# Optimization experiments

Measured on AMD Instinct MI355X. Metric: run time of the kernel, lower is better.

Reference implementation:

```python
import jax, jax.numpy as jnp
import numpy as np

N, M, FEAT, GROUP, EMB = 512, 2048, 1024, 16, 64
DG = FEAT // GROUP  # 64 dims per head


def _make_boxes(k, n):
    k1, k2, k3, k4 = jax.random.split(k, 4)
    x = jax.random.uniform(k1, (n, 1)) * 800.0
    y = jax.random.uniform(k2, (n, 1)) * 800.0
    w = jax.random.uniform(k3, (n, 1)) * 120.0 + 16.0
    h = jax.random.uniform(k4, (n, 1)) * 120.0 + 16.0
    return jnp.concatenate([x, y, x + w, y + h], axis=1)


def setup_inputs() -> dict:
    key = jax.random.key(0)
    ks = jax.random.split(key, 10)
    std = 0.01
    fan = 1.0 / np.sqrt(FEAT).astype(np.float32)
    return {
        "bbox": _make_boxes(ks[0], N),
        "ref_bbox": _make_boxes(ks[1], M),
        "roi_feat": jax.random.normal(ks[2], (N, FEAT), dtype=jnp.float32),
        "ref_feat": jax.random.normal(ks[3], (M, FEAT), dtype=jnp.float32),
        "Wg_w": jax.random.normal(ks[4], (GROUP, EMB)) * std,
        "Wg_b": jnp.zeros((GROUP,), jnp.float32),
        "Wq_w": jax.random.normal(ks[5], (FEAT, FEAT)) * fan,
        "Wq_b": jnp.zeros((FEAT,), jnp.float32),
        "Wk_w": jax.random.normal(ks[6], (FEAT, FEAT)) * fan,
        "Wk_b": jnp.zeros((FEAT,), jnp.float32),
        "Wv_w": jax.random.normal(ks[7], (GROUP, DG, FEAT)) * std,
        "Wv_b": jnp.zeros((FEAT,), jnp.float32),
        "u": jax.random.normal(ks[8], (GROUP, 1, EMB)) * std,
    }


def _position_embedding(bbox, ref_bbox, feat_dim=64, wave_length=1000.0):
    # extract_position_matrix: geometry deltas between every (roi, ref) pair
    xr0, yr0, xr1, yr1 = jnp.split(ref_bbox, 4, axis=1)  # [M,1]
    wr = xr1 - xr0 + 1.0
    hr = yr1 - yr0 + 1.0
    cxr = 0.5 * (xr0 + xr1)
    cyr = 0.5 * (yr0 + yr1)
    x0, y0, x1, y1 = jnp.split(bbox, 4, axis=1)  # [N,1]
    w = x1 - x0 + 1.0
    h = y1 - y0 + 1.0
    cx = 0.5 * (x0 + x1)
    cy = 0.5 * (y0 + y1)
    dx = jnp.log(jnp.abs((cx - cxr.T) / w) + 1e-3)  # [N,M]
    dy = jnp.log(jnp.abs((cy - cyr.T) / h) + 1e-3)
    dw = jnp.log(w / wr.T)
    dh = jnp.log(h / hr.T)
    pos = jnp.stack([dx, dy, dw, dh], axis=2)  # [N,M,4]
    # extract_position_embedding: sinusoidal encoding, feat_dim/8 frequencies
    fr = jnp.arange(feat_dim // 8, dtype=pos.dtype)
    dim_mat = wave_length ** (8.0 / feat_dim * fr)  # [8]
    div = (pos[..., None] * 100.0) / dim_mat  # [N,M,4,8]
    emb = jnp.concatenate([jnp.sin(div), jnp.cos(div)], axis=3)  # [N,M,4,16]
    emb = emb.reshape(emb.shape[0], emb.shape[1], -1)  # [N,M,64]
    return jnp.transpose(emb, (2, 0, 1))  # [emb_dim, N, M]


def reference(bbox, ref_bbox, roi_feat, ref_feat, Wg_w, Wg_b, Wq_w, Wq_b,
              Wk_w, Wk_b, Wv_w, Wv_b, u):
    pe = _position_embedding(bbox, ref_bbox)  # [EMB, N, M]
    # Wg: 1x1 conv over embedding channels, relu -> attention prior weights
    pos_feat = jax.nn.relu(jnp.einsum('ge,enm->gnm', Wg_w, pe)
                           + Wg_b[:, None, None])  # [G,N,M]
    aff_weight = jnp.transpose(pos_feat, (1, 0, 2))  # [N,G,M]
    q = (roi_feat @ Wq_w.T + Wq_b).reshape(-1, GROUP, DG).transpose(1, 0, 2)  # [G,N,DG]
    k = (ref_feat @ Wk_w.T + Wk_b).reshape(-1, GROUP, DG).transpose(1, 0, 2)  # [G,M,DG]
    # content score + global content-bias (u) score, per head
    aff = jnp.einsum('gnd,gmd->gnm', q, k) + jnp.einsum('gld,gmd->glm', u, k)
    aff_scale = (aff / np.sqrt(float(DG))).transpose(1, 0, 2)  # [N,G,M]
    weighted_aff = jnp.log(aff_weight + 1e-6) + aff_scale
    attn = jax.nn.softmax(weighted_aff, axis=2)  # [N,G,M]
    out_t = jnp.einsum('ngm,mf->ngf', attn, ref_feat)  # [N,G,FEAT]
    # grouped 1x1 conv Wv: per-group weight [DG, FEAT]
    out = jnp.einsum('ngc,gdc->ngd', out_t, Wv_w).reshape(-1, FEAT) + Wv_b
    return out  # [N, FEAT]
```

## Files before the change

kernel.cpp:

```cpp
#include <hip/hip_runtime.h>
#include <stdint.h>

typedef float f32x4 __attribute__((ext_vector_type(4)));
typedef _Float16 f16x8 __attribute__((ext_vector_type(8)));
typedef _Float16 f16x4 __attribute__((ext_vector_type(4)));
typedef int int4v __attribute__((ext_vector_type(4)));

#define LOG2E 1.44269504088896340736f

__device__ __forceinline__ void gload_lds16(const void* g, void* l) {
    auto gp = reinterpret_cast<const uint32_t __attribute__((address_space(1)))*>(
        reinterpret_cast<uintptr_t>(g));
    auto lp = reinterpret_cast<uint32_t __attribute__((address_space(3)))*>(
        reinterpret_cast<uintptr_t>(l));
    __builtin_amdgcn_global_load_lds(gp, lp, 16, 0, 0);
}

__global__ __launch_bounds__(256) void mega_prep(
    const float* __restrict__ roi_feat, const float* __restrict__ ref_feat,
    const float* __restrict__ Wg_w, const float* __restrict__ Wq_w,
    const float* __restrict__ Wk_w, const float* __restrict__ Wv_w,
    _Float16* __restrict__ roi_h, _Float16* __restrict__ ref_h,
    _Float16* __restrict__ wq_h, _Float16* __restrict__ wk_h,
    _Float16* __restrict__ wv_h, _Float16* __restrict__ wg_h)
{
    int idx = blockIdx.x * 256 + threadIdx.x;
    const float* src; _Float16* dst; int off;
    if (idx < 131072)       { src = roi_feat; dst = roi_h; off = idx; }
    else if (idx < 655360)  { src = ref_feat; dst = ref_h; off = idx - 131072; }
    else if (idx < 917504)  { src = Wq_w;     dst = wq_h;  off = idx - 655360; }
    else if (idx < 1179648) { src = Wk_w;     dst = wk_h;  off = idx - 917504; }
    else if (idx < 1441792) { src = Wv_w;     dst = wv_h;  off = idx - 1179648; }
    else                    { src = Wg_w;     dst = wg_h;  off = idx - 1441792; }
    f32x4 v = *(const f32x4*)(src + (size_t)off * 4);
    f16x4 o;
    o[0] = (_Float16)v[0]; o[1] = (_Float16)v[1];
    o[2] = (_Float16)v[2]; o[3] = (_Float16)v[3];
    *(f16x4*)(dst + (size_t)off * 4) = o;
}

__global__ __launch_bounds__(256, 4) void mega_gp(
    const _Float16* __restrict__ roi_h, const _Float16* __restrict__ ref_h,
    const _Float16* __restrict__ wq_h, const _Float16* __restrict__ wk_h,
    const _Float16* __restrict__ wv_h, const _Float16* __restrict__ wg_h,
    const float* __restrict__ Wq_b, const float* __restrict__ uvec,
    const float* __restrict__ Wk_b, const float* __restrict__ Wg_b,
    const float* __restrict__ bbox, const float* __restrict__ ref_bbox,
    _Float16* __restrict__ Qg, _Float16* __restrict__ Kg, _Float16* __restrict__ Vth,
    _Float16* __restrict__ prior)
{
    __shared__ __align__(16) _Float16 As[2][4096];
    __shared__ __align__(16) _Float16 Bs[2][4096];

    int b = blockIdx.x;
    int tid = threadIdx.x;
    int w = tid >> 6, l = tid & 63, q = l >> 4, t = l & 15;

    if (b >= 1152) {
        int pb = b - 1152;
        int p = l & 15;
        int n = pb >> 1, half = pb & 1;

        f16x8 wa0 = *(const f16x8*)(wg_h + p*64 + q*8);
        f16x8 wa1 = *(const f16x8*)(wg_h + p*64 + 32 + q*8);
        f32x4 wb = *(const f32x4*)(Wg_b + q*4);

        f32x4 bbx = *(const f32x4*)(bbox + n * 4);
        float bw = bbx[2] - bbx[0] + 1.0f, bh = bbx[3] - bbx[1] + 1.0f;
        float cx = 0.5f*(bbx[0]+bbx[2]), cy = 0.5f*(bbx[1]+bbx[3]);
        float invw = 1.0f/bw, invh = 1.0f/bh;
        float lgw = __logf(bw), lgh = __logf(bh);

        float cf[8];
        #pragma unroll
        for (int f = 0; f < 8; ++f)
            cf[f] = 15.9154943091895336f * __builtin_exp2f(-1.24572303558276059f * (float)f);

        float coff = (q & 1) ? 0.25f : 0.0f;
        bool isX = (q < 2);
        float cA  = isX ? cx : cy;
        float invA = isX ? invw : invh;
        float lgA = isX ? lgw : lgh;

        int mstart = half * 1024 + w * 256;
        for (int it = 0; it < 16; ++it) {
            int m = mstart + it * 16 + p;
            f32x4 rb = *(const f32x4*)(ref_bbox + m * 4);
            float cAr = isX ? 0.5f*(rb[0]+rb[2]) : 0.5f*(rb[1]+rb[3]);
            float sAr = isX ? (rb[2]-rb[0]+1.0f) : (rb[3]-rb[1]+1.0f);
            float posA = __logf(fabsf(cA - cAr) * invA + 1e-3f);
            float posB = lgA - __logf(sAr);
            f16x8 e0, e1;
            #pragma unroll
            for (int f = 0; f < 8; ++f) {
                float a0 = posA * cf[f] + coff; a0 -= floorf(a0);
                float a1 = posB * cf[f] + coff; a1 -= floorf(a1);
                e0[f] = (_Float16)__builtin_amdgcn_sinf(a0);
                e1[f] = (_Float16)__builtin_amdgcn_sinf(a1);
            }
            f32x4 acc = wb;
            acc = __builtin_amdgcn_mfma_f32_16x16x32_f16(wa0, e0, acc, 0, 0, 0);
            acc = __builtin_amdgcn_mfma_f32_16x16x32_f16(wa1, e1, acc, 0, 0, 0);
            _Float16* pp = prior + (size_t)n * 2048 + m;
            #pragma unroll
            for (int r = 0; r < 4; ++r)
                pp[(size_t)(q*4 + r) * 1048576] = (_Float16)fmaxf(acc[r], 0.f);
        }
        return;
    }

    const _Float16 *A, *B;
    _Float16* out;
    int tm, tn, mode; float scale;
    if (b < 128)      { A = roi_h; B = wq_h; out = Qg;  tm = b >> 4;        tn = b & 15;       mode = 0; scale = 0.125f * LOG2E; }
    else if (b < 640) { A = ref_h; B = wk_h; out = Kg;  tm = (b-128) >> 4;  tn = (b-128) & 15; mode = 1; scale = 1.f; }
    else              { A = ref_h; B = wv_h; out = Vth; tm = (b-640) >> 4;  tn = (b-640) & 15; mode = 2; scale = 1.f; }
    int MR = (b < 128) ? 512 : 2048;

    int wm = w >> 1, wn = w & 1;
    int m0 = tm * 64, n0 = tn * 64;

    int r_lo = tid >> 3, c8 = tid & 7;
    int swz = (c8 * 16) ^ ((r_lo & 7) << 4);
    const char* gA = (const char*)A + (size_t)(m0 + r_lo) * 2048 + swz;
    const char* gB = (const char*)B + (size_t)(n0 + r_lo) * 2048 + swz;
    char* lA = (char*)&As[0][0] + w * 1024;
    char* lB = (char*)&Bs[0][0] + w * 1024;

#define GSTAGE(bufi, kt) { \
    size_t ko = (size_t)(kt) * 128; \
    gload_lds16(gA + ko,           lA + (bufi)*8192); \
    gload_lds16(gA + ko + 32*2048, lA + (bufi)*8192 + 4096); \
    gload_lds16(gB + ko,           lB + (bufi)*8192); \
    gload_lds16(gB + ko + 32*2048, lB + (bufi)*8192 + 4096); }

    f32x4 acc[2][2];
    #pragma unroll
    for (int i = 0; i < 2; ++i)
        #pragma unroll
        for (int j = 0; j < 2; ++j)
            acc[i][j] = (f32x4){0.f, 0.f, 0.f, 0.f};

    GSTAGE(0, 0);
    __syncthreads();

    for (int kt = 0; kt < 16; ++kt) {
        int cur = kt & 1;
        if (kt < 15) GSTAGE(cur ^ 1, kt + 1);

        const char* cA = (const char*)&As[0][0] + cur * 8192;
        const char* cB = (const char*)&Bs[0][0] + cur * 8192;
        f16x8 af[2][2], bf[2][2];
        #pragma unroll
        for (int mi = 0; mi < 2; ++mi) {
            int row = wm * 32 + mi * 16 + t;
            int sx = (row & 7) << 4;
            #pragma unroll
            for (int ks = 0; ks < 2; ++ks)
                af[ks][mi] = *(const f16x8*)(cA + row * 128 + ((ks * 64 + q * 16) ^ sx));
        }
        #pragma unroll
        for (int ni = 0; ni < 2; ++ni) {
            int row = wn * 32 + ni * 16 + t;
            int sx = (row & 7) << 4;
            #pragma unroll
            for (int ks = 0; ks < 2; ++ks)
                bf[ks][ni] = *(const f16x8*)(cB + row * 128 + ((ks * 64 + q * 16) ^ sx));
        }
        #pragma unroll
        for (int ks = 0; ks < 2; ++ks)
            #pragma unroll
            for (int mi = 0; mi < 2; ++mi)
                #pragma unroll
                for (int ni = 0; ni < 2; ++ni)
                    acc[mi][ni] = __builtin_amdgcn_mfma_f32_16x16x32_f16(af[ks][mi], bf[ks][ni], acc[mi][ni], 0, 0, 0);
        __syncthreads();
    }
#undef GSTAGE

    #pragma unroll
    for (int mi = 0; mi < 2; ++mi) {
        #pragma unroll
        for (int ni = 0; ni < 2; ++ni) {
            int col  = n0 + wn*32 + ni*16 + t;
            int row0 = m0 + wm*32 + mi*16 + q*4;
            f32x4 a = acc[mi][ni];
            if (mode == 2) {
                f16x4 pk;
                pk[0] = (_Float16)a[0]; pk[1] = (_Float16)a[1];
                pk[2] = (_Float16)a[2]; pk[3] = (_Float16)a[3];
                *(f16x4*)(out + (size_t)col * 2048 + row0) = pk;
            } else {
                float bb = (mode == 0) ? (Wq_b[col] + uvec[col]) : Wk_b[col];
                _Float16* op = out + ((size_t)(col >> 6) * MR + row0) * 64 + (col & 63);
                #pragma unroll
                for (int rr = 0; rr < 4; ++rr)
                    op[(size_t)rr * 64] = (_Float16)((a[rr] + bb) * scale);
            }
        }
    }
}

#define SWZ(row, cb) ((cb) ^ (((row) & 7) << 4))

__device__ __forceinline__ f16x8 ld128s(const _Float16* base, int row, int cb) {
    return *(const f16x8*)((const char*)base + row * 128 + SWZ(row, cb));
}
__device__ __forceinline__ f16x4 ld64s(const _Float16* base, int row, int cb) {
    return *(const f16x4*)((const char*)base + row * 128 + SWZ(row, cb));
}

__global__ __launch_bounds__(256, 3) void mega_attn(
    const _Float16* __restrict__ Qg, const _Float16* __restrict__ Kg,
    const _Float16* __restrict__ Vth, const _Float16* __restrict__ prior,
    _Float16* __restrict__ Opart, float* __restrict__ Mpart, float* __restrict__ Lpart)
{
    __shared__ __align__(16) _Float16 Kl[2][4096];
    __shared__ __align__(16) _Float16 Vl[2][4096];
    __shared__ __align__(16) _Float16 Pl[2][4096];

    int bid = blockIdx.x;
    int g = bid >> 6, nt4 = (bid >> 3) & 7, s = bid & 7;
    int tid = threadIdx.x;
    int w = tid >> 6, l = tid & 63, q = l >> 4, t = l & 15;
    int n0 = nt4 * 64, m0 = s * 256;

    int n = n0 + w * 16 + t;
    const _Float16* Qrow = Qg + ((size_t)g * 512 + n) * 64;
    f16x8 qf0 = *(const f16x8*)(Qrow + q * 8);
    f16x8 qf1 = *(const f16x8*)(Qrow + 32 + q * 8);

    int r_lo = tid >> 3, c8 = tid & 7;
    const char* gK = (const char*)(Kg + ((size_t)g * 2048 + m0) * 64);
    const char* gV = (const char*)(Vth + (size_t)g * 64 * 2048 + m0);
    const char* gP = (const char*)(prior + ((size_t)g * 512 + n0) * 2048 + m0);

    int4v kr0, kr1, vr0, vr1, pq0, pq1;
#define LOADC(c) { \
    kr0 = *(const int4v*)(gK + (c)*8192 + r_lo*128 + c8*16); \
    kr1 = *(const int4v*)(gK + (c)*8192 + (r_lo+32)*128 + c8*16); \
    vr0 = *(const int4v*)(gV + (c)*128 + (size_t)r_lo*4096 + c8*16); \
    vr1 = *(const int4v*)(gV + (c)*128 + (size_t)(r_lo+32)*4096 + c8*16); \
    pq0 = *(const int4v*)(gP + (c)*128 + (size_t)r_lo*4096 + c8*16); \
    pq1 = *(const int4v*)(gP + (c)*128 + (size_t)(r_lo+32)*4096 + c8*16); }
#define WRITEC(bufi) { \
    int cb = c8 * 16, sw = SWZ(r_lo, cb); \
    *(int4v*)((char*)&Kl[bufi][0] + r_lo*128 + sw) = kr0; \
    *(int4v*)((char*)&Kl[bufi][0] + (r_lo+32)*128 + sw) = kr1; \
    *(int4v*)((char*)&Vl[bufi][0] + r_lo*128 + sw) = vr0; \
    *(int4v*)((char*)&Vl[bufi][0] + (r_lo+32)*128 + sw) = vr1; \
    *(int4v*)((char*)&Pl[bufi][0] + r_lo*128 + sw) = pq0; \
    *(int4v*)((char*)&Pl[bufi][0] + (r_lo+32)*128 + sw) = pq1; }

    float mrow = -INFINITY, lsum = 0.f;
    f32x4 O0 = {0,0,0,0}, O1 = {0,0,0,0}, O2 = {0,0,0,0}, O3 = {0,0,0,0};

    LOADC(0);
    WRITEC(0);
    __syncthreads();

    for (int c = 0; c < 4; ++c) {
        int cur = c & 1;
        if (c < 3) LOADC(c + 1);

        const _Float16* Kb_l = &Kl[cur][0];
        const _Float16* Vb_l = &Vl[cur][0];
        const _Float16* Pb_l = &Pl[cur][0];

        f16x4 pr[4];
        #pragma unroll
        for (int mi = 0; mi < 4; ++mi)
            pr[mi] = ld64s(Pb_l, w * 16 + t, mi * 32 + q * 8);
        f32x4 sv[4];
        __builtin_amdgcn_s_setprio(1);
        #pragma unroll
        for (int mi = 0; mi < 4; ++mi) {
            f16x8 k0 = ld128s(Kb_l, mi * 16 + t, q * 16);
            f16x8 k1 = ld128s(Kb_l, mi * 16 + t, 64 + q * 16);
            f32x4 z = {0, 0, 0, 0};
            z = __builtin_amdgcn_mfma_f32_16x16x32_f16(k0, qf0, z, 0, 0, 0);
            z = __builtin_amdgcn_mfma_f32_16x16x32_f16(k1, qf1, z, 0, 0, 0);
            sv[mi] = z;
        }
        __builtin_amdgcn_s_setprio(0);
        #pragma unroll
        for (int mi = 0; mi < 4; ++mi)
            #pragma unroll
            for (int r = 0; r < 4; ++r)
                sv[mi][r] += __log2f((float)pr[mi][r] + 1e-6f);
        f16x4 vv[4][4];
        #pragma unroll
        for (int i = 0; i < 4; ++i)
            #pragma unroll
            for (int mi = 0; mi < 4; ++mi)
                vv[i][mi] = ld64s(Vb_l, i * 16 + t, mi * 32 + q * 8);
        float cmax = -INFINITY;
        #pragma unroll
        for (int mi = 0; mi < 4; ++mi)
            #pragma unroll
            for (int r = 0; r < 4; ++r)
                cmax = fmaxf(cmax, sv[mi][r]);
        cmax = fmaxf(cmax, __shfl_xor(cmax, 16));
        cmax = fmaxf(cmax, __shfl_xor(cmax, 32));
        float mnew = fmaxf(mrow, cmax);
        float corr = __builtin_exp2f(mrow - mnew);
        float psum = 0.f;
        f16x4 pf[4];
        #pragma unroll
        for (int mi = 0; mi < 4; ++mi) {
            #pragma unroll
            for (int r = 0; r < 4; ++r) {
                float pv = __builtin_exp2f(sv[mi][r] - mnew);
                psum += pv;
                pf[mi][r] = (_Float16)pv;
            }
        }
        psum += __shfl_xor(psum, 16);
        psum += __shfl_xor(psum, 32);
        lsum = lsum * corr + psum;
        mrow = mnew;
        O0 *= corr; O1 *= corr; O2 *= corr; O3 *= corr;
        __builtin_amdgcn_s_setprio(1);
        #pragma unroll
        for (int mi = 0; mi < 4; ++mi) {
            O0 = __builtin_amdgcn_mfma_f32_16x16x16f16(vv[0][mi], pf[mi], O0, 0, 0, 0);
            O1 = __builtin_amdgcn_mfma_f32_16x16x16f16(vv[1][mi], pf[mi], O1, 0, 0, 0);
            O2 = __builtin_amdgcn_mfma_f32_16x16x16f16(vv[2][mi], pf[mi], O2, 0, 0, 0);
            O3 = __builtin_amdgcn_mfma_f32_16x16x16f16(vv[3][mi], pf[mi], O3, 0, 0, 0);
        }
        __builtin_amdgcn_s_setprio(0);

        if (c < 3) WRITEC(cur ^ 1);
        __syncthreads();
    }

    int u = ((g * 32 + nt4 * 4 + w) << 3) + s;
    size_t ob = (size_t)(u * 16 + t) * 64;
    f16x4 ph;
#define PK(O) { ph[0]=(_Float16)O[0]; ph[1]=(_Float16)O[1]; ph[2]=(_Float16)O[2]; ph[3]=(_Float16)O[3]; }
    PK(O0) *(f16x4*)(Opart + ob + q*4)      = ph;
    PK(O1) *(f16x4*)(Opart + ob + 16 + q*4) = ph;
    PK(O2) *(f16x4*)(Opart + ob + 32 + q*4) = ph;
    PK(O3) *(f16x4*)(Opart + ob + 48 + q*4) = ph;
#undef PK
    if (q == 0) { Mpart[u*16 + t] = mrow; Lpart[u*16 + t] = lsum; }
#undef LOADC
#undef WRITEC
}

__global__ __launch_bounds__(256) void mega_combine(
    const _Float16* __restrict__ Opart, const float* __restrict__ Mpart,
    const float* __restrict__ Lpart, const float* __restrict__ Wv_b,
    float* __restrict__ outp)
{
    int idx = blockIdx.x * 256 + threadIdx.x;
    int n = idx >> 10, col = idx & 1023;
    int g = col >> 6, d = col & 63;
    int nt = n >> 4, t = n & 15;
    int u0 = ((g * 32 + nt) << 3);
    float ms[8];
    #pragma unroll
    for (int s = 0; s < 8; ++s) ms[s] = Mpart[(u0 + s) * 16 + t];
    float M = ms[0];
    #pragma unroll
    for (int s = 1; s < 8; ++s) M = fmaxf(M, ms[s]);
    float accO = 0.f, accL = 0.f;
    #pragma unroll
    for (int s = 0; s < 8; ++s) {
        float wgt = __builtin_exp2f(ms[s] - M);
        accO += wgt * (float)Opart[(size_t)((u0 + s) * 16 + t) * 64 + d];
        accL += wgt * Lpart[(u0 + s) * 16 + t];
    }
    outp[idx] = accO / accL + Wv_b[col];
}

extern "C" void kernel_launch(void* const* d_in, const int* in_sizes, int n_in,
                              void* d_out, int out_size, void* d_ws, size_t ws_size,
                              hipStream_t stream)
{
    const float* bbox     = (const float*)d_in[0];
    const float* ref_bbox = (const float*)d_in[1];
    const float* roi_feat = (const float*)d_in[2];
    const float* ref_feat = (const float*)d_in[3];
    const float* Wg_w = (const float*)d_in[4];
    const float* Wg_b = (const float*)d_in[5];
    const float* Wq_w = (const float*)d_in[6];
    const float* Wq_b = (const float*)d_in[7];
    const float* Wk_w = (const float*)d_in[8];
    const float* Wk_b = (const float*)d_in[9];
    const float* Wv_w = (const float*)d_in[10];
    const float* Wv_b = (const float*)d_in[11];
    const float* uvec = (const float*)d_in[12];
    float* outp = (float*)d_out;
    char* ws = (char*)d_ws;

    _Float16* roi_h = (_Float16*)(ws + 0);
    _Float16* ref_h = (_Float16*)(ws + (1ull<<20));
    _Float16* wq_h  = (_Float16*)(ws + (5ull<<20));
    _Float16* wk_h  = (_Float16*)(ws + (7ull<<20));
    _Float16* wv_h  = (_Float16*)(ws + (9ull<<20));
    _Float16* wg_h  = (_Float16*)(ws + (11ull<<20));
    size_t b2 = 12ull<<20;
    _Float16* prior = (_Float16*)(ws + b2);
    size_t b3 = b2 + (32ull<<20);
    _Float16* Qh    = (_Float16*)(ws + b3);
    _Float16* Kh    = (_Float16*)(ws + b3 + (1ull<<20));
    _Float16* Vth   = (_Float16*)(ws + b3 + (5ull<<20));
    _Float16* Opart = (_Float16*)(ws + b3 + (9ull<<20));
    float* Mpart    = (float*)(ws + b3 + (25ull<<20));
    float* Lpart    = (float*)(ws + b3 + (25ull<<20) + 262144);

    mega_prep<<<5633, 256, 0, stream>>>(roi_feat, ref_feat,
        Wg_w, Wq_w, Wk_w, Wv_w,
        roi_h, ref_h, wq_h, wk_h, wv_h, wg_h);
    mega_gp<<<2176, 256, 0, stream>>>(roi_h, ref_h, wq_h, wk_h, wv_h, wg_h,
        Wq_b, uvec, Wk_b, Wg_b, bbox, ref_bbox,
        Qh, Kh, Vth, prior);
    mega_attn<<<1024, 256, 0, stream>>>(Qh, Kh, Vth, prior, Opart, Mpart, Lpart);
    mega_combine<<<2048, 256, 0, stream>>>(Opart, Mpart, Lpart, Wv_b, outp);
}
```

Baseline: 146.9 us.

## Split projection GEMM from prior kernel, enlarge GEMM and attention tiles

Moves the positional-prior computation out of the fused GEMM kernel into its own launch. The Q/K/V projection GEMM tiles grow from 64x64 to 128x128 with a 4x4 MFMA accumulator per wave, and the MFMA loop runs at raised priority. Attention blocks double to 512 threads covering 128 query rows, and V/prior fragments are loaded just before use instead of being held in registers. The aim is more reuse per staged tile and lower register pressure, at the cost of fewer GEMM blocks (288 on a large GPU), an extra launch, and serialised prior/GEMM execution.

Result: slower. 154.8 us (+5.4%).

```diff
diff --git a/kernel.cpp b/kernel.cpp
--- a/kernel.cpp
+++ b/kernel.cpp
@@ -39,106 +39,54 @@
     *(f16x4*)(dst + (size_t)off * 4) = o;
 }
 
-__global__ __launch_bounds__(256, 4) void mega_gp(
+__global__ __launch_bounds__(256, 2) void mega_gemm(
     const _Float16* __restrict__ roi_h, const _Float16* __restrict__ ref_h,
     const _Float16* __restrict__ wq_h, const _Float16* __restrict__ wk_h,
-    const _Float16* __restrict__ wv_h, const _Float16* __restrict__ wg_h,
+    const _Float16* __restrict__ wv_h,
     const float* __restrict__ Wq_b, const float* __restrict__ uvec,
-    const float* __restrict__ Wk_b, const float* __restrict__ Wg_b,
-    const float* __restrict__ bbox, const float* __restrict__ ref_bbox,
-    _Float16* __restrict__ Qg, _Float16* __restrict__ Kg, _Float16* __restrict__ Vth,
-    _Float16* __restrict__ prior)
-{
-    __shared__ __align__(16) _Float16 As[2][4096];
-    __shared__ __align__(16) _Float16 Bs[2][4096];
+    const float* __restrict__ Wk_b,
+    _Float16* __restrict__ Qg, _Float16* __restrict__ Kg, _Float16* __restrict__ Vth)
+{
+    __shared__ __align__(16) _Float16 As[2][128 * 64];
+    __shared__ __align__(16) _Float16 Bs[2][128 * 64];
 
     int b = blockIdx.x;
-    int tid = threadIdx.x;
-    int w = tid >> 6, l = tid & 63, q = l >> 4, t = l & 15;
-
-    if (b >= 1152) {
-        int pb = b - 1152;
-        int p = l & 15;
-        int n = pb >> 1, half = pb & 1;
-
-        f16x8 wa0 = *(const f16x8*)(wg_h + p*64 + q*8);
-        f16x8 wa1 = *(const f16x8*)(wg_h + p*64 + 32 + q*8);
-        f32x4 wb = *(const f32x4*)(Wg_b + q*4);
-
-        f32x4 bbx = *(const f32x4*)(bbox + n * 4);
-        float bw = bbx[2] - bbx[0] + 1.0f, bh = bbx[3] - bbx[1] + 1.0f;
-        float cx = 0.5f*(bbx[0]+bbx[2]), cy = 0.5f*(bbx[1]+bbx[3]);
-        float invw = 1.0f/bw, invh = 1.0f/bh;
-        float lgw = __logf(bw), lgh = __logf(bh);
-
-        float cf[8];
-        #pragma unroll
-        for (int f = 0; f < 8; ++f)
-            cf[f] = 15.9154943091895336f * __builtin_exp2f(-1.24572303558276059f * (float)f);
-
-        float coff = (q & 1) ? 0.25f : 0.0f;
-        bool isX = (q < 2);
-        float cA  = isX ? cx : cy;
-        float invA = isX ? invw : invh;
-        float lgA = isX ? lgw : lgh;
-
-        int mstart = half * 1024 + w * 256;
-        for (int it = 0; it < 16; ++it) {
-            int m = mstart + it * 16 + p;
-            f32x4 rb = *(const f32x4*)(ref_bbox + m * 4);
-            float cAr = isX ? 0.5f*(rb[0]+rb[2]) : 0.5f*(rb[1]+rb[3]);
-            float sAr = isX ? (rb[2]-rb[0]+1.0f) : (rb[3]-rb[1]+1.0f);
-            float posA = __logf(fabsf(cA - cAr) * invA + 1e-3f);
-            float posB = lgA - __logf(sAr);
-            f16x8 e0, e1;
-            #pragma unroll
-            for (int f = 0; f < 8; ++f) {
-                float a0 = posA * cf[f] + coff; a0 -= floorf(a0);
-                float a1 = posB * cf[f] + coff; a1 -= floorf(a1);
-                e0[f] = (_Float16)__builtin_amdgcn_sinf(a0);
-                e1[f] = (_Float16)__builtin_amdgcn_sinf(a1);
-            }
-            f32x4 acc = wb;
-            acc = __builtin_amdgcn_mfma_f32_16x16x32_f16(wa0, e0, acc, 0, 0, 0);
-            acc = __builtin_amdgcn_mfma_f32_16x16x32_f16(wa1, e1, acc, 0, 0, 0);
-            _Float16* pp = prior + (size_t)n * 2048 + m;
-            #pragma unroll
-            for (int r = 0; r < 4; ++r)
-                pp[(size_t)(q*4 + r) * 1048576] = (_Float16)fmaxf(acc[r], 0.f);
-        }
-        return;
-    }
-
     const _Float16 *A, *B;
     _Float16* out;
     int tm, tn, mode; float scale;
-    if (b < 128)      { A = roi_h; B = wq_h; out = Qg;  tm = b >> 4;        tn = b & 15;       mode = 0; scale = 0.125f * LOG2E; }
-    else if (b < 640) { A = ref_h; B = wk_h; out = Kg;  tm = (b-128) >> 4;  tn = (b-128) & 15; mode = 1; scale = 1.f; }
-    else              { A = ref_h; B = wv_h; out = Vth; tm = (b-640) >> 4;  tn = (b-640) & 15; mode = 2; scale = 1.f; }
-    int MR = (b < 128) ? 512 : 2048;
-
+    if (b < 32)       { A = roi_h; B = wq_h; out = Qg;  tm = b >> 3;        tn = b & 7;       mode = 0; scale = 0.125f * LOG2E; }
+    else if (b < 160) { A = ref_h; B = wk_h; out = Kg;  tm = (b-32) >> 3;   tn = (b-32) & 7;  mode = 1; scale = 1.f; }
+    else              { A = ref_h; B = wv_h; out = Vth; tm = (b-160) >> 3;  tn = (b-160) & 7; mode = 2; scale = 1.f; }
+    int MR = (b < 32) ? 512 : 2048;
+
+    int tid = threadIdx.x;
+    int w = tid >> 6, l = tid & 63, q = l >> 4, t = l & 15;
     int wm = w >> 1, wn = w & 1;
-    int m0 = tm * 64, n0 = tn * 64;
+    int m0 = tm * 128, n0 = tn * 128;
 
     int r_lo = tid >> 3, c8 = tid & 7;
     int swz = (c8 * 16) ^ ((r_lo & 7) << 4);
     const char* gA = (const char*)A + (size_t)(m0 + r_lo) * 2048 + swz;
     const char* gB = (const char*)B + (size_t)(n0 + r_lo) * 2048 + swz;
-    char* lA = (char*)&As[0][0] + w * 1024;
-    char* lB = (char*)&Bs[0][0] + w * 1024;
+    char* lA = (char*)&As[0][0] + (w * 8) * 128;
+    char* lB = (char*)&Bs[0][0] + (w * 8) * 128;
 
 #define GSTAGE(bufi, kt) { \
     size_t ko = (size_t)(kt) * 128; \
-    gload_lds16(gA + ko,           lA + (bufi)*8192); \
-    gload_lds16(gA + ko + 32*2048, lA + (bufi)*8192 + 4096); \
-    gload_lds16(gB + ko,           lB + (bufi)*8192); \
-    gload_lds16(gB + ko + 32*2048, lB + (bufi)*8192 + 4096); }
-
-    f32x4 acc[2][2];
-    #pragma unroll
-    for (int i = 0; i < 2; ++i)
-        #pragma unroll
-        for (int j = 0; j < 2; ++j)
+    gload_lds16(gA + ko,           lA + (bufi)*16384); \
+    gload_lds16(gA + ko + 32*2048, lA + (bufi)*16384 + 4096); \
+    gload_lds16(gA + ko + 64*2048, lA + (bufi)*16384 + 8192); \
+    gload_lds16(gA + ko + 96*2048, lA + (bufi)*16384 + 12288); \
+    gload_lds16(gB + ko,           lB + (bufi)*16384); \
+    gload_lds16(gB + ko + 32*2048, lB + (bufi)*16384 + 4096); \
+    gload_lds16(gB + ko + 64*2048, lB + (bufi)*16384 + 8192); \
+    gload_lds16(gB + ko + 96*2048, lB + (bufi)*16384 + 12288); }
+
+    f32x4 acc[4][4];
+    #pragma unroll
+    for (int i = 0; i < 4; ++i)
+        #pragma unroll
+        for (int j = 0; j < 4; ++j)
             acc[i][j] = (f32x4){0.f, 0.f, 0.f, 0.f};
 
     GSTAGE(0, 0);
@@ -148,42 +96,44 @@
         int cur = kt & 1;
         if (kt < 15) GSTAGE(cur ^ 1, kt + 1);
 
-        const char* cA = (const char*)&As[0][0] + cur * 8192;
-        const char* cB = (const char*)&Bs[0][0] + cur * 8192;
-        f16x8 af[2][2], bf[2][2];
-        #pragma unroll
-        for (int mi = 0; mi < 2; ++mi) {
-            int row = wm * 32 + mi * 16 + t;
+        const char* cA = (const char*)&As[0][0] + cur * 16384;
+        const char* cB = (const char*)&Bs[0][0] + cur * 16384;
+        f16x8 af[2][4], bf[2][4];
+        #pragma unroll
+        for (int mi = 0; mi < 4; ++mi) {
+            int row = wm * 64 + mi * 16 + t;
             int sx = (row & 7) << 4;
             #pragma unroll
             for (int ks = 0; ks < 2; ++ks)
                 af[ks][mi] = *(const f16x8*)(cA + row * 128 + ((ks * 64 + q * 16) ^ sx));
         }
         #pragma unroll
-        for (int ni = 0; ni < 2; ++ni) {
-            int row = wn * 32 + ni * 16 + t;
+        for (int ni = 0; ni < 4; ++ni) {
+            int row = wn * 64 + ni * 16 + t;
             int sx = (row & 7) << 4;
             #pragma unroll
             for (int ks = 0; ks < 2; ++ks)
                 bf[ks][ni] = *(const f16x8*)(cB + row * 128 + ((ks * 64 + q * 16) ^ sx));
         }
+        __builtin_amdgcn_s_setprio(1);
         #pragma unroll
         for (int ks = 0; ks < 2; ++ks)
             #pragma unroll
-            for (int mi = 0; mi < 2; ++mi)
+            for (int mi = 0; mi < 4; ++mi)
                 #pragma unroll
-                for (int ni = 0; ni < 2; ++ni)
+                for (int ni = 0; ni < 4; ++ni)
                     acc[mi][ni] = __builtin_amdgcn_mfma_f32_16x16x32_f16(af[ks][mi], bf[ks][ni], acc[mi][ni], 0, 0, 0);
+        __builtin_amdgcn_s_setprio(0);
         __syncthreads();
     }
 #undef GSTAGE
 
     #pragma unroll
-    for (int mi = 0; mi < 2; ++mi) {
-        #pragma unroll
-        for (int ni = 0; ni < 2; ++ni) {
-            int col  = n0 + wn*32 + ni*16 + t;
-            int row0 = m0 + wm*32 + mi*16 + q*4;
+    for (int mi = 0; mi < 4; ++mi) {
+        #pragma unroll
+        for (int ni = 0; ni < 4; ++ni) {
+            int col  = n0 + wn*64 + ni*16 + t;
+            int row0 = m0 + wm*64 + mi*16 + q*4;
             f32x4 a = acc[mi][ni];
             if (mode == 2) {
                 f16x4 pk;
@@ -201,6 +151,60 @@
     }
 }
 
+__global__ __launch_bounds__(256) void mega_prior(
+    const _Float16* __restrict__ wg_h, const float* __restrict__ Wg_b,
+    const float* __restrict__ bbox, const float* __restrict__ ref_bbox,
+    _Float16* __restrict__ prior)
+{
+    int tid = threadIdx.x;
+    int w = tid >> 6, l = tid & 63, q = l >> 4, p = l & 15;
+    int n = blockIdx.x >> 1, half = blockIdx.x & 1;
+
+    f16x8 wa0 = *(const f16x8*)(wg_h + p*64 + q*8);
+    f16x8 wa1 = *(const f16x8*)(wg_h + p*64 + 32 + q*8);
+    f32x4 wb = *(const f32x4*)(Wg_b + q*4);
+
+    f32x4 bbx = *(const f32x4*)(bbox + n * 4);
+    float bw = bbx[2] - bbx[0] + 1.0f, bh = bbx[3] - bbx[1] + 1.0f;
+    float cx = 0.5f*(bbx[0]+bbx[2]), cy = 0.5f*(bbx[1]+bbx[3]);
+
+    float cf[8];
+    #pragma unroll
+    for (int f = 0; f < 8; ++f)
+        cf[f] = 15.9154943091895336f * __builtin_exp2f(-1.24572303558276059f * (float)f);
+
+    float coff = (q & 1) ? 0.25f : 0.0f;
+    bool isX = (q < 2);
+    float cA   = isX ? cx : cy;
+    float invA = isX ? 1.0f/bw : 1.0f/bh;
+    float lgA  = isX ? __logf(bw) : __logf(bh);
+
+    int mstart = half * 1024 + w * 256;
+    for (int it = 0; it < 16; ++it) {
+        int m = mstart + it * 16 + p;
+        f32x4 rb = *(const f32x4*)(ref_bbox + m * 4);
+        float cAr = isX ? 0.5f*(rb[0]+rb[2]) : 0.5f*(rb[1]+rb[3]);
+        float sAr = isX ? (rb[2]-rb[0]+1.0f) : (rb[3]-rb[1]+1.0f);
+        float posA = __logf(fabsf(cA - cAr) * invA + 1e-3f);
+        float posB = lgA - __logf(sAr);
+        f16x8 e0, e1;
+        #pragma unroll
+        for (int f = 0; f < 8; ++f) {
+            float a0 = posA * cf[f] + coff; a0 -= floorf(a0);
+            float a1 = posB * cf[f] + coff; a1 -= floorf(a1);
+            e0[f] = (_Float16)__builtin_amdgcn_sinf(a0);
+            e1[f] = (_Float16)__builtin_amdgcn_sinf(a1);
+        }
+        f32x4 acc = wb;
+        acc = __builtin_amdgcn_mfma_f32_16x16x32_f16(wa0, e0, acc, 0, 0, 0);
+        acc = __builtin_amdgcn_mfma_f32_16x16x32_f16(wa1, e1, acc, 0, 0, 0);
+        _Float16* pp = prior + (size_t)n * 2048 + m;
+        #pragma unroll
+        for (int r = 0; r < 4; ++r)
+            pp[(size_t)(q*4 + r) * 1048576] = (_Float16)fmaxf(acc[r], 0.f);
+    }
+}
+
 #define SWZ(row, cb) ((cb) ^ (((row) & 7) << 4))
 
 __device__ __forceinline__ f16x8 ld128s(const _Float16* base, int row, int cb) {
@@ -210,20 +214,20 @@
     return *(const f16x4*)((const char*)base + row * 128 + SWZ(row, cb));
 }
 
-__global__ __launch_bounds__(256, 3) void mega_attn(
+__global__ __launch_bounds__(512, 4) void mega_attn(
     const _Float16* __restrict__ Qg, const _Float16* __restrict__ Kg,
     const _Float16* __restrict__ Vth, const _Float16* __restrict__ prior,
     _Float16* __restrict__ Opart, float* __restrict__ Mpart, float* __restrict__ Lpart)
 {
     __shared__ __align__(16) _Float16 Kl[2][4096];
     __shared__ __align__(16) _Float16 Vl[2][4096];
-    __shared__ __align__(16) _Float16 Pl[2][4096];
+    __shared__ __align__(16) _Float16 Pl[2][8192];
 
     int bid = blockIdx.x;
-    int g = bid >> 6, nt4 = (bid >> 3) & 7, s = bid & 7;
+    int g = bid >> 5, nt2 = (bid >> 3) & 3, s = bid & 7;
     int tid = threadIdx.x;
     int w = tid >> 6, l = tid & 63, q = l >> 4, t = l & 15;
-    int n0 = nt4 * 64, m0 = s * 256;
+    int n0 = nt2 * 128, m0 = s * 256;
 
     int n = n0 + w * 16 + t;
     const _Float16* Qrow = Qg + ((size_t)g * 512 + n) * 64;
@@ -235,25 +239,21 @@
     const char* gV = (const char*)(Vth + (size_t)g * 64 * 2048 + m0);
     const char* gP = (const char*)(prior + ((size_t)g * 512 + n0) * 2048 + m0);
 
-    int4v kr0, kr1, vr0, vr1, pq0, pq1;
+    int4v kr, vr, pq0, pq1;
 #define LOADC(c) { \
-    kr0 = *(const int4v*)(gK + (c)*8192 + r_lo*128 + c8*16); \
-    kr1 = *(const int4v*)(gK + (c)*8192 + (r_lo+32)*128 + c8*16); \
-    vr0 = *(const int4v*)(gV + (c)*128 + (size_t)r_lo*4096 + c8*16); \
-    vr1 = *(const int4v*)(gV + (c)*128 + (size_t)(r_lo+32)*4096 + c8*16); \
+    kr  = *(const int4v*)(gK + (c)*8192 + r_lo*128 + c8*16); \
+    vr  = *(const int4v*)(gV + (c)*128 + (size_t)r_lo*4096 + c8*16); \
     pq0 = *(const int4v*)(gP + (c)*128 + (size_t)r_lo*4096 + c8*16); \
-    pq1 = *(const int4v*)(gP + (c)*128 + (size_t)(r_lo+32)*4096 + c8*16); }
+    pq1 = *(const int4v*)(gP + (c)*128 + (size_t)(r_lo+64)*4096 + c8*16); }
 #define WRITEC(bufi) { \
-    int cb = c8 * 16, sw = SWZ(r_lo, cb); \
-    *(int4v*)((char*)&Kl[bufi][0] + r_lo*128 + sw) = kr0; \
-    *(int4v*)((char*)&Kl[bufi][0] + (r_lo+32)*128 + sw) = kr1; \
-    *(int4v*)((char*)&Vl[bufi][0] + r_lo*128 + sw) = vr0; \
-    *(int4v*)((char*)&Vl[bufi][0] + (r_lo+32)*128 + sw) = vr1; \
+    int sw = SWZ(r_lo, c8 * 16); \
+    *(int4v*)((char*)&Kl[bufi][0] + r_lo*128 + sw) = kr; \
+    *(int4v*)((char*)&Vl[bufi][0] + r_lo*128 + sw) = vr; \
     *(int4v*)((char*)&Pl[bufi][0] + r_lo*128 + sw) = pq0; \
-    *(int4v*)((char*)&Pl[bufi][0] + (r_lo+32)*128 + sw) = pq1; }
+    *(int4v*)((char*)&Pl[bufi][0] + (r_lo+64)*128 + sw) = pq1; }
 
     float mrow = -INFINITY, lsum = 0.f;
-    f32x4 O0 = {0,0,0,0}, O1 = {0,0,0,0}, O2 = {0,0,0,0}, O3 = {0,0,0,0};
+    f32x4 Ov[4] = {{0,0,0,0},{0,0,0,0},{0,0,0,0},{0,0,0,0}};
 
     LOADC(0);
     WRITEC(0);
@@ -267,10 +267,6 @@
         const _Float16* Vb_l = &Vl[cur][0];
         const _Float16* Pb_l = &Pl[cur][0];
 
-        f16x4 pr[4];
-        #pragma unroll
-        for (int mi = 0; mi < 4; ++mi)
-            pr[mi] = ld64s(Pb_l, w * 16 + t, mi * 32 + q * 8);
         f32x4 sv[4];
         __builtin_amdgcn_s_setprio(1);
         #pragma unroll
@@ -284,16 +280,12 @@
         }
         __builtin_amdgcn_s_setprio(0);
         #pragma unroll
-        for (int mi = 0; mi < 4; ++mi)
+        for (int mi = 0; mi < 4; ++mi) {
+            f16x4 pr = ld64s(Pb_l, w * 16 + t, mi * 32 + q * 8);
             #pragma unroll
             for (int r = 0; r < 4; ++r)
-                sv[mi][r] += __log2f((float)pr[mi][r] + 1e-6f);
-        f16x4 vv[4][4];
-        #pragma unroll
-        for (int i = 0; i < 4; ++i)
-            #pragma unroll
-            for (int mi = 0; mi < 4; ++mi)
-                vv[i][mi] = ld64s(Vb_l, i * 16 + t, mi * 32 + q * 8);
+                sv[mi][r] += __log2f((float)pr[r] + 1e-6f);
+        }
         float cmax = -INFINITY;
         #pragma unroll
         for (int mi = 0; mi < 4; ++mi)
@@ -319,14 +311,16 @@
         psum += __shfl_xor(psum, 32);
         lsum = lsum * corr + psum;
         mrow = mnew;
-        O0 *= corr; O1 *= corr; O2 *= corr; O3 *= corr;
+        #pragma unroll
+        for (int i = 0; i < 4; ++i) Ov[i] *= corr;
         __builtin_amdgcn_s_setprio(1);
         #pragma unroll
-        for (int mi = 0; mi < 4; ++mi) {
-            O0 = __builtin_amdgcn_mfma_f32_16x16x16f16(vv[0][mi], pf[mi], O0, 0, 0, 0);
-            O1 = __builtin_amdgcn_mfma_f32_16x16x16f16(vv[1][mi], pf[mi], O1, 0, 0, 0);
-            O2 = __builtin_amdgcn_mfma_f32_16x16x16f16(vv[2][mi], pf[mi], O2, 0, 0, 0);
-            O3 = __builtin_amdgcn_mfma_f32_16x16x16f16(vv[3][mi], pf[mi], O3, 0, 0, 0);
+        for (int i = 0; i < 4; ++i) {
+            #pragma unroll
+            for (int mi = 0; mi < 4; ++mi) {
+                f16x4 vv = ld64s(Vb_l, i * 16 + t, mi * 32 + q * 8);
+                Ov[i] = __builtin_amdgcn_mfma_f32_16x16x16f16(vv, pf[mi], Ov[i], 0, 0, 0);
+            }
         }
         __builtin_amdgcn_s_setprio(0);
 
@@ -334,15 +328,15 @@
         __syncthreads();
     }
 
-    int u = ((g * 32 + nt4 * 4 + w) << 3) + s;
+    int u = ((g * 32 + nt2 * 8 + w) << 3) + s;
     size_t ob = (size_t)(u * 16 + t) * 64;
-    f16x4 ph;
-#define PK(O) { ph[0]=(_Float16)O[0]; ph[1]=(_Float16)O[1]; ph[2]=(_Float16)O[2]; ph[3]=(_Float16)O[3]; }
-    PK(O0) *(f16x4*)(Opart + ob + q*4)      = ph;
-    PK(O1) *(f16x4*)(Opart + ob + 16 + q*4) = ph;
-    PK(O2) *(f16x4*)(Opart + ob + 32 + q*4) = ph;
-    PK(O3) *(f16x4*)(Opart + ob + 48 + q*4) = ph;
-#undef PK
+    #pragma unroll
+    for (int i = 0; i < 4; ++i) {
+        f16x4 ph;
+        ph[0] = (_Float16)Ov[i][0]; ph[1] = (_Float16)Ov[i][1];
+        ph[2] = (_Float16)Ov[i][2]; ph[3] = (_Float16)Ov[i][3];
+        *(f16x4*)(Opart + ob + i * 16 + q * 4) = ph;
+    }
     if (q == 0) { Mpart[u*16 + t] = mrow; Lpart[u*16 + t] = lsum; }
 #undef LOADC
 #undef WRITEC
@@ -413,9 +407,9 @@
     mega_prep<<<5633, 256, 0, stream>>>(roi_feat, ref_feat,
         Wg_w, Wq_w, Wk_w, Wv_w,
         roi_h, ref_h, wq_h, wk_h, wv_h, wg_h);
-    mega_gp<<<2176, 256, 0, stream>>>(roi_h, ref_h, wq_h, wk_h, wv_h, wg_h,
-        Wq_b, uvec, Wk_b, Wg_b, bbox, ref_bbox,
-        Qh, Kh, Vth, prior);
-    mega_attn<<<1024, 256, 0, stream>>>(Qh, Kh, Vth, prior, Opart, Mpart, Lpart);
+    mega_gemm<<<288, 256, 0, stream>>>(roi_h, ref_h, wq_h, wk_h, wv_h,
+        Wq_b, uvec, Wk_b, Qh, Kh, Vth);
+    mega_prior<<<1024, 256, 0, stream>>>(wg_h, Wg_b, bbox, ref_bbox, prior);
+    mega_attn<<<512, 512, 0, stream>>>(Qh, Kh, Vth, prior, Opart, Mpart, Lpart);
     mega_combine<<<2048, 256, 0, stream>>>(Opart, Mpart, Lpart, Wv_b, outp);
 }
```
